# Optimization experiments

Hardware: AMD Instinct MI355X
Metric: run time of the kernel (lower is better)

## Reference

```python
import jax, jax.numpy as jnp
import numpy as np

EPS = 1e-5
NUM_HEADS = 16


def _layernorm(x, g, b):
    mu = jnp.mean(x, axis=-1, keepdims=True)
    var = jnp.mean(jnp.square(x - mu), axis=-1, keepdims=True)
    return (x - mu) * jax.lax.rsqrt(var + EPS) * g + b


def setup_inputs() -> dict:
    key = jax.random.key(0)
    ks = jax.random.split(key, 8)
    B, N, D, Hid = 2, 2048, 1024, 4096
    s = 0.02
    return {
        "x": jax.random.normal(ks[0], (B, N, D), dtype=jnp.float32),
        "w_qkv": jax.random.normal(ks[1], (D, 3 * D), dtype=jnp.float32) * s,
        "b_qkv": jnp.zeros((3 * D,), dtype=jnp.float32),
        "ln_g": jnp.ones((D,), dtype=jnp.float32),
        "ln_b": jnp.zeros((D,), dtype=jnp.float32),
        "w1": jax.random.normal(ks[2], (D, Hid), dtype=jnp.float32) * s,
        "b1": jnp.zeros((Hid,), dtype=jnp.float32),
        "w2": jax.random.normal(ks[3], (Hid, D), dtype=jnp.float32) * s,
        "b2": jnp.zeros((D,), dtype=jnp.float32),
    }


def reference(x, w_qkv, b_qkv, ln_g, ln_b, w1, b1, w2, b2):
    B, N, D = x.shape
    H = NUM_HEADS
    Dh = D // H

    # --- attention branch (pre-norm, shared LayerNorm params) ---
    xn = _layernorm(x, ln_g, ln_b)
    qkv = xn @ w_qkv + b_qkv                       # [B, N, 3D]
    qkv = qkv.reshape(B, N, 3, H, Dh).transpose(2, 0, 3, 1, 4)  # [3, B, H, N, Dh]
    q, k, v = qkv[0], qkv[1], qkv[2]
    # NOTE: original module applies NO 1/sqrt(Dh) scaling
    att = jax.nn.softmax(jnp.einsum('bhqd,bhkd->bhqk', q, k), axis=-1)
    o = jnp.einsum('bhqk,bhkd->bhqd', att, v)      # [B, H, N, Dh]
    # Faithful to source: raw reshape of [B, H, N, Dh] -> [B, N, D]
    # (the original code does NOT transpose heads back before merging)
    attn_out = o.reshape(B, N, D)
    x = x + attn_out

    # --- MLP branch ---
    xn2 = _layernorm(x, ln_g, ln_b)
    h = jax.nn.gelu(xn2 @ w1 + b1, approximate=False)
    mlp_out = h @ w2 + b2
    return x + mlp_out
```

## Files before the change

### kernel.cpp

```cpp
#include <hip/hip_runtime.h>
#include <cstdint>
#include <math.h>

typedef __attribute__((ext_vector_type(4))) float f32x4;
typedef __attribute__((ext_vector_type(8))) short bf16x8;
typedef unsigned short u16;
typedef __attribute__((ext_vector_type(4))) unsigned short u16x4;

#define LOG2E 1.44269504088896340736f

__device__ __forceinline__ u16 f2bf(float f) {
  uint32_t u = __builtin_bit_cast(uint32_t, f);
  u += 0x7FFFu + ((u >> 16) & 1u);
  return (u16)(u >> 16);
}

__device__ __forceinline__ void g2lds16(const void* g, void* l) {
  __builtin_amdgcn_global_load_lds((const __attribute__((address_space(1))) void*)g,
                                   (__attribute__((address_space(3))) void*)l, 16, 0, 0);
}

__device__ __forceinline__ float qsum16(float v) {
  v += __shfl_xor(v, 1);
  v += __shfl_xor(v, 2);
  v += __shfl_xor(v, 4);
  v += __shfl_xor(v, 8);
  return v;
}
__device__ __forceinline__ float wsum64(float v) {
  #pragma unroll
  for (int m = 32; m > 0; m >>= 1) v += __shfl_xor(v, m);
  return v;
}

__global__ void __launch_bounds__(256) transpose_f32_bf16(
    const float* __restrict__ in, u16* __restrict__ out, int R, int C) {
  __shared__ float tile[32][33];
  const int bx = blockIdx.x, by = blockIdx.y;
  const int tx = threadIdx.x & 31, ty = threadIdx.x >> 5;
  #pragma unroll
  for (int j = 0; j < 4; ++j)
    tile[ty + j * 8][tx] = in[(size_t)(by * 32 + ty + j * 8) * C + bx * 32 + tx];
  __syncthreads();
  #pragma unroll
  for (int j = 0; j < 4; ++j)
    out[(size_t)(bx * 32 + ty + j * 8) * R + by * 32 + tx] = f2bf(tile[tx][ty + j * 8]);
}

__global__ void __launch_bounds__(256) ln_kernel(
    const float* __restrict__ x, const float* __restrict__ g,
    const float* __restrict__ b, u16* __restrict__ out) {
  __shared__ float red[8];
  const int row = blockIdx.x, t = threadIdx.x, w = t >> 6;
  const float4 v = ((const float4*)(x + (size_t)row * 1024))[t];
  float s = v.x + v.y + v.z + v.w;
  s = wsum64(s);
  if ((t & 63) == 0) red[w] = s;
  __syncthreads();
  const float mean = (red[0] + red[1] + red[2] + red[3]) * (1.0f / 1024.0f);
  const float dx = v.x - mean, dy = v.y - mean, dz = v.z - mean, dw = v.w - mean;
  float s2 = dx * dx + dy * dy + dz * dz + dw * dw;
  s2 = wsum64(s2);
  if ((t & 63) == 0) red[4 + w] = s2;
  __syncthreads();
  const float rstd = rsqrtf((red[4] + red[5] + red[6] + red[7]) * (1.0f / 1024.0f) + 1e-5f);
  const float4 gv = ((const float4*)g)[t];
  const float4 bv = ((const float4*)b)[t];
  u16x4 o;
  o.x = f2bf(dx * rstd * gv.x + bv.x);
  o.y = f2bf(dy * rstd * gv.y + bv.y);
  o.z = f2bf(dz * rstd * gv.z + bv.z);
  o.w = f2bf(dw * rstd * gv.w + bv.w);
  ((u16x4*)(out + (size_t)row * 1024))[t] = o;
}

template <int EPI>
__global__ void __launch_bounds__(256, 2) gemm_bt(
    const u16* __restrict__ A, const u16* __restrict__ Bt,
    const float* __restrict__ bias, int M, int N, int K,
    u16* __restrict__ ob) {
  __shared__ u16 As[128 * 32];
  __shared__ u16 Bs[128 * 32];
  const int t = threadIdx.x;
  const int w = t >> 6, l = t & 63;
  const int lq = l >> 4, lr = l & 15;
  const int sw = (lr >> 1) & 3;
  const int wm = w >> 1, wn = w & 1;
  const int row0 = blockIdx.x * 128, col0 = blockIdx.y * 128;
  f32x4 acc[4][4] = {};
  for (int k0 = 0; k0 < K; k0 += 32) {
    #pragma unroll
    for (int i = 0; i < 2; ++i) {
      int c = i * 256 + t;
      int row = c >> 2, cl = (c & 3) ^ ((row >> 1) & 3);
      g2lds16(A + (size_t)(row0 + row) * K + k0 + cl * 8,
              (char*)As + (i * 256 + w * 64) * 16);
    }
    #pragma unroll
    for (int i = 0; i < 2; ++i) {
      int c = i * 256 + t;
      int row = c >> 2, cl = (c & 3) ^ ((row >> 1) & 3);
      g2lds16(Bt + (size_t)(col0 + row) * K + k0 + cl * 8,
              (char*)Bs + (i * 256 + w * 64) * 16);
    }
    __syncthreads();
    bf16x8 af[4], bf[4];
    #pragma unroll
    for (int tm = 0; tm < 4; ++tm)
      af[tm] = *(const bf16x8*)&As[(wm * 64 + tm * 16 + lr) * 32 + (lq ^ sw) * 8];
    #pragma unroll
    for (int tn = 0; tn < 4; ++tn)
      bf[tn] = *(const bf16x8*)&Bs[(wn * 64 + tn * 16 + lr) * 32 + (lq ^ sw) * 8];
    #pragma unroll
    for (int tm = 0; tm < 4; ++tm)
      #pragma unroll
      for (int tn = 0; tn < 4; ++tn)
        acc[tm][tn] = __builtin_amdgcn_mfma_f32_16x16x32_bf16(af[tm], bf[tn], acc[tm][tn], 0, 0, 0);
    __syncthreads();
  }
  #pragma unroll
  for (int tm = 0; tm < 4; ++tm) {
    #pragma unroll
    for (int tn = 0; tn < 4; ++tn) {
      const int gcol = col0 + wn * 64 + tn * 16 + lr;
      const float bv = bias[gcol];
      float vals[4];
      #pragma unroll
      for (int r = 0; r < 4; ++r) vals[r] = acc[tm][tn][r] + bv;
      const int g0 = row0 + wm * 64 + tm * 16 + lq * 4;
      if (EPI == 0) {
        const int tsel = gcol >> 10, hh = (gcol >> 6) & 15, dh = gcol & 63;
        const int bb = g0 >> 11, n0 = g0 & 2047;
        if (tsel == 2) {
          u16x4 pk;
          pk.x = f2bf(vals[0]); pk.y = f2bf(vals[1]);
          pk.z = f2bf(vals[2]); pk.w = f2bf(vals[3]);
          *(u16x4*)&ob[8388608 + (size_t)((bb * 16 + hh) * 64 + dh) * 2048 + n0] = pk;
        } else {
          const float sc = (tsel == 0) ? LOG2E : 1.0f;
          const size_t base = (tsel ? 4194304u : 0u) +
                              (size_t)(bb * 16 + hh) * 2048 * 64 + dh;
          #pragma unroll
          for (int r = 0; r < 4; ++r)
            ob[base + (size_t)(n0 + r) * 64] = f2bf(vals[r] * sc);
        }
      } else {
        #pragma unroll
        for (int r = 0; r < 4; ++r) {
          const float gelu = 0.5f * vals[r] * (1.0f + erff(vals[r] * 0.70710678118654752f));
          ob[(size_t)(g0 + r) * N + gcol] = f2bf(gelu);
        }
      }
    }
  }
}

__global__ void __launch_bounds__(256) gemm2_db(
    const u16* __restrict__ A, const u16* __restrict__ Bt,
    const float* __restrict__ bias, const float* __restrict__ res,
    float* __restrict__ of) {
  __shared__ u16 As0[128 * 128], As1[128 * 128];
  __shared__ u16 Bs0[128 * 128], Bs1[128 * 128];
  const int t = threadIdx.x;
  const int w = t >> 6, l = t & 63;
  const int lq = l >> 4, lr = l & 15;
  const int sw = lr & 7;
  const int wm = w >> 1, wn = w & 1;
  const int row0 = blockIdx.x * 128, col0 = blockIdx.y * 128;
  const int K = 4096, N = 1024;

#define STAGE(kt, AS, BS)                                                  \
  {                                                                        \
    _Pragma("unroll")                                                      \
    for (int i = 0; i < 8; ++i) {                                          \
      int c = i * 256 + t;                                                 \
      int row = c >> 4, cl = (c & 15) ^ (row & 7);                         \
      g2lds16(A + (size_t)(row0 + row) * K + (kt) * 128 + cl * 8,          \
              (char*)(AS) + (i * 256 + w * 64) * 16);                      \
    }                                                                      \
    _Pragma("unroll")                                                      \
    for (int i = 0; i < 8; ++i) {                                          \
      int c = i * 256 + t;                                                 \
      int row = c >> 4, cl = (c & 15) ^ (row & 7);                         \
      g2lds16(Bt + (size_t)(col0 + row) * K + (kt) * 128 + cl * 8,         \
              (char*)(BS) + (i * 256 + w * 64) * 16);                      \
    }                                                                      \
  }

#define COMPUTE(AS, BS)                                                    \
  {                                                                        \
    _Pragma("unroll")                                                      \
    for (int kk = 0; kk < 4; ++kk) {                                       \
      bf16x8 af[4], bf[4];                                                 \
      _Pragma("unroll")                                                    \
      for (int tm = 0; tm < 4; ++tm)                                       \
        af[tm] = *(const bf16x8*)&(AS)[(wm * 64 + tm * 16 + lr) * 128 +    \
                                       (((kk * 4 + lq) ^ sw)) * 8];        \
      _Pragma("unroll")                                                    \
      for (int tn = 0; tn < 4; ++tn)                                       \
        bf[tn] = *(const bf16x8*)&(BS)[(wn * 64 + tn * 16 + lr) * 128 +    \
                                       (((kk * 4 + lq) ^ sw)) * 8];        \
      _Pragma("unroll")                                                    \
      for (int tm = 0; tm < 4; ++tm)                                       \
        _Pragma("unroll")                                                  \
        for (int tn = 0; tn < 4; ++tn)                                     \
          acc[tm][tn] = __builtin_amdgcn_mfma_f32_16x16x32_bf16(           \
              af[tm], bf[tn], acc[tm][tn], 0, 0, 0);                       \
    }                                                                      \
  }

  f32x4 acc[4][4] = {};
  STAGE(0, As0, Bs0);
  for (int kt = 0; kt < 32; kt += 2) {
    __syncthreads();
    STAGE(kt + 1, As1, Bs1);
    COMPUTE(As0, Bs0);
    __syncthreads();
    if (kt + 2 < 32) STAGE(kt + 2, As0, Bs0);
    COMPUTE(As1, Bs1);
  }
#undef STAGE
#undef COMPUTE

  #pragma unroll
  for (int tm = 0; tm < 4; ++tm) {
    #pragma unroll
    for (int tn = 0; tn < 4; ++tn) {
      const int gcol = col0 + wn * 64 + tn * 16 + lr;
      const float bv = bias[gcol];
      const int g0 = row0 + wm * 64 + tm * 16 + lq * 4;
      #pragma unroll
      for (int r = 0; r < 4; ++r) {
        const size_t idx = (size_t)(g0 + r) * N + gcol;
        of[idx] = res[idx] + acc[tm][tn][r] + bv;
      }
    }
  }
}

__global__ void __launch_bounds__(256, 2) attn_kernel(
    const u16* __restrict__ q, const u16* __restrict__ k, const u16* __restrict__ vt,
    const float* __restrict__ x, float* __restrict__ x2) {
  __shared__ u16 Ks[128 * 64];
  __shared__ u16 Vs[64 * 128];
  __shared__ u16 Ps[4][16 * 136];
  const int t = threadIdx.x, w = t >> 6, l = t & 63;
  const int lq = l >> 4, lr = l & 15;
  const int sw = lr & 7;
  const int bh = blockIdx.y, qt = blockIdx.x;
  const size_t head = (size_t)bh * (2048 * 64);
  const u16* qh = q + head;
  const u16* kh = k + head;
  const u16* vth = vt + head;

  bf16x8 qf[2][2];
  #pragma unroll
  for (int tm = 0; tm < 2; ++tm)
    #pragma unroll
    for (int kk = 0; kk < 2; ++kk)
      qf[tm][kk] = *(const bf16x8*)&qh[(size_t)(qt * 128 + w * 32 + tm * 16 + lr) * 64 + kk * 32 + lq * 8];

  f32x4 o_acc[2][4] = {};
  float rsum[2][4] = {};
  u16* const pbase = &Ps[w][lq * 544 + lr];

  for (int kt = 0; kt < 16; ++kt) {
    #pragma unroll
    for (int i = 0; i < 4; ++i) {
      int c = i * 256 + t;
      int row = c >> 3, cl = (c & 7) ^ (row & 7);
      g2lds16(kh + (size_t)(kt * 128 + row) * 64 + cl * 8,
              (char*)Ks + (i * 256 + w * 64) * 16);
    }
    #pragma unroll
    for (int i = 0; i < 4; ++i) {
      int c = i * 256 + t;
      int row = c >> 4, cl = (c & 15) ^ (row & 7);
      g2lds16(vth + (size_t)row * 2048 + kt * 128 + cl * 8,
              (char*)Vs + (i * 256 + w * 64) * 16);
    }
    __syncthreads();
    bf16x8 kf[8][2];
    #pragma unroll
    for (int tn = 0; tn < 8; ++tn)
      #pragma unroll
      for (int kk = 0; kk < 2; ++kk)
        kf[tn][kk] = *(const bf16x8*)&Ks[(tn * 16 + lr) * 64 + ((kk * 4 + lq) ^ sw) * 8];
    #pragma unroll
    for (int tm = 0; tm < 2; ++tm) {
      f32x4 s_acc[8] = {};
      #pragma unroll
      for (int tn = 0; tn < 8; ++tn)
        #pragma unroll
        for (int kk = 0; kk < 2; ++kk)
          s_acc[tn] = __builtin_amdgcn_mfma_f32_16x16x32_bf16(qf[tm][kk], kf[tn][kk], s_acc[tn], 0, 0, 0);
      #pragma unroll
      for (int tn = 0; tn < 8; ++tn)
        #pragma unroll
        for (int r = 0; r < 4; ++r) {
          const float p = __builtin_amdgcn_exp2f(s_acc[tn][r]);
          rsum[tm][r] += p;
          pbase[r * 136 + tn * 16] = (u16)(__builtin_bit_cast(uint32_t, p) >> 16);
        }
      #pragma unroll
      for (int kk2 = 0; kk2 < 4; ++kk2) {
        const bf16x8 pf = *(const bf16x8*)&Ps[w][lr * 136 + kk2 * 32 + lq * 8];
        #pragma unroll
        for (int tn = 0; tn < 4; ++tn) {
          const bf16x8 vf = *(const bf16x8*)&Vs[(tn * 16 + lr) * 128 + ((kk2 * 4 + lq) ^ sw) * 8];
          o_acc[tm][tn] = __builtin_amdgcn_mfma_f32_16x16x32_bf16(pf, vf, o_acc[tm][tn], 0, 0, 0);
        }
      }
    }
    __syncthreads();
  }
  float inv[2][4];
  #pragma unroll
  for (int tm = 0; tm < 2; ++tm)
    #pragma unroll
    for (int r = 0; r < 4; ++r)
      inv[tm][r] = 1.0f / qsum16(rsum[tm][r]);
  const int bb = bh >> 4, hh = bh & 15;
  const size_t base = (size_t)bb * 2097152 + (size_t)hh * 131072;
  #pragma unroll
  for (int tm = 0; tm < 2; ++tm)
    #pragma unroll
    for (int tn = 0; tn < 4; ++tn)
      #pragma unroll
      for (int r = 0; r < 4; ++r) {
        const int n = qt * 128 + w * 32 + tm * 16 + lq * 4 + r;
        const int dh = tn * 16 + lr;
        const size_t idx = base + (size_t)n * 64 + dh;
        x2[idx] = x[idx] + o_acc[tm][tn][r] * inv[tm][r];
      }
}

extern "C" void kernel_launch(void* const* d_in, const int* in_sizes, int n_in,
                              void* d_out, int out_size, void* d_ws, size_t ws_size,
                              hipStream_t stream) {
  const float* x     = (const float*)d_in[0];
  const float* w_qkv = (const float*)d_in[1];
  const float* b_qkv = (const float*)d_in[2];
  const float* ln_g  = (const float*)d_in[3];
  const float* ln_b  = (const float*)d_in[4];
  const float* w1    = (const float*)d_in[5];
  const float* b1    = (const float*)d_in[6];
  const float* w2    = (const float*)d_in[7];
  const float* b2    = (const float*)d_in[8];
  float* out = (float*)d_out;
  char* ws = (char*)d_ws;

  u16*  wqkvT = (u16*)(ws + 0);
  u16*  qb    = (u16*)(ws + 6291456);
  u16*  xn    = (u16*)(ws + 31457280);
  u16*  h     = (u16*)(ws + 0);
  float* x2   = (float*)(ws + 39845888);
  u16*  w1T   = (u16*)(ws + 56623104);
  u16*  w2T   = (u16*)(ws + 65011712);
  u16*  xn2   = (u16*)(ws + 73400320);

  transpose_f32_bf16<<<dim3(3072 / 32, 1024 / 32), 256, 0, stream>>>(w_qkv, wqkvT, 1024, 3072);
  transpose_f32_bf16<<<dim3(4096 / 32, 1024 / 32), 256, 0, stream>>>(w1, w1T, 1024, 4096);
  transpose_f32_bf16<<<dim3(1024 / 32, 4096 / 32), 256, 0, stream>>>(w2, w2T, 4096, 1024);

  ln_kernel<<<4096, 256, 0, stream>>>(x, ln_g, ln_b, xn);
  gemm_bt<0><<<dim3(32, 24), 256, 0, stream>>>(xn, wqkvT, b_qkv, 4096, 3072, 1024, qb);
  attn_kernel<<<dim3(16, 32), 256, 0, stream>>>(qb, qb + 4194304, qb + 8388608, x, x2);
  ln_kernel<<<4096, 256, 0, stream>>>(x2, ln_g, ln_b, xn2);
  gemm_bt<1><<<dim3(32, 32), 256, 0, stream>>>(xn2, w1T, b1, 4096, 4096, 1024, h);
  gemm2_db<<<dim3(32, 8), 256, 0, stream>>>(h, w2T, b2, x2, out);
}
```

Measured before the change: 318.8 us.

## Double-buffer K/V tiles in attention kernel with smaller 64-key tiles

The attention loop now works on 64-key tiles instead of 128 and keeps two LDS buffers for K and V. The next tile's async global-to-LDS loads are issued before computing on the current one, so load latency overlaps MFMA and exp work. The P scratch row stride changes from 136 to 132, and P is read back as two 8-byte loads. This costs more barriers per key, and smaller tiles mean less work between each synchronisation.

```diff
diff --git a/kernel.cpp b/kernel.cpp
--- a/kernel.cpp
+++ b/kernel.cpp
@@ -4,6 +4,7 @@
 
 typedef __attribute__((ext_vector_type(4))) float f32x4;
 typedef __attribute__((ext_vector_type(8))) short bf16x8;
+typedef __attribute__((ext_vector_type(4))) short s16x4;
 typedef unsigned short u16;
 typedef __attribute__((ext_vector_type(4))) unsigned short u16x4;
 
@@ -241,9 +242,9 @@
 __global__ void __launch_bounds__(256, 2) attn_kernel(
     const u16* __restrict__ q, const u16* __restrict__ k, const u16* __restrict__ vt,
     const float* __restrict__ x, float* __restrict__ x2) {
-  __shared__ u16 Ks[128 * 64];
-  __shared__ u16 Vs[64 * 128];
-  __shared__ u16 Ps[4][16 * 136];
+  __shared__ u16 Ks0[64 * 64], Ks1[64 * 64];
+  __shared__ u16 Vs0[64 * 64], Vs1[64 * 64];
+  __shared__ u16 Ps[4][16 * 132];
   const int t = threadIdx.x, w = t >> 6, l = t & 63;
   const int lq = l >> 4, lr = l & 15;
   const int sw = lr & 7;
@@ -262,58 +263,79 @@
 
   f32x4 o_acc[2][4] = {};
   float rsum[2][4] = {};
-  u16* const pbase = &Ps[w][lq * 544 + lr];
-
-  for (int kt = 0; kt < 16; ++kt) {
-    #pragma unroll
-    for (int i = 0; i < 4; ++i) {
-      int c = i * 256 + t;
-      int row = c >> 3, cl = (c & 7) ^ (row & 7);
-      g2lds16(kh + (size_t)(kt * 128 + row) * 64 + cl * 8,
-              (char*)Ks + (i * 256 + w * 64) * 16);
-    }
-    #pragma unroll
-    for (int i = 0; i < 4; ++i) {
-      int c = i * 256 + t;
-      int row = c >> 4, cl = (c & 15) ^ (row & 7);
-      g2lds16(vth + (size_t)row * 2048 + kt * 128 + cl * 8,
-              (char*)Vs + (i * 256 + w * 64) * 16);
-    }
-    __syncthreads();
-    bf16x8 kf[8][2];
-    #pragma unroll
-    for (int tn = 0; tn < 8; ++tn)
-      #pragma unroll
-      for (int kk = 0; kk < 2; ++kk)
-        kf[tn][kk] = *(const bf16x8*)&Ks[(tn * 16 + lr) * 64 + ((kk * 4 + lq) ^ sw) * 8];
-    #pragma unroll
-    for (int tm = 0; tm < 2; ++tm) {
-      f32x4 s_acc[8] = {};
-      #pragma unroll
-      for (int tn = 0; tn < 8; ++tn)
-        #pragma unroll
-        for (int kk = 0; kk < 2; ++kk)
-          s_acc[tn] = __builtin_amdgcn_mfma_f32_16x16x32_bf16(qf[tm][kk], kf[tn][kk], s_acc[tn], 0, 0, 0);
-      #pragma unroll
-      for (int tn = 0; tn < 8; ++tn)
-        #pragma unroll
-        for (int r = 0; r < 4; ++r) {
-          const float p = __builtin_amdgcn_exp2f(s_acc[tn][r]);
-          rsum[tm][r] += p;
-          pbase[r * 136 + tn * 16] = (u16)(__builtin_bit_cast(uint32_t, p) >> 16);
-        }
-      #pragma unroll
-      for (int kk2 = 0; kk2 < 4; ++kk2) {
-        const bf16x8 pf = *(const bf16x8*)&Ps[w][lr * 136 + kk2 * 32 + lq * 8];
-        #pragma unroll
-        for (int tn = 0; tn < 4; ++tn) {
-          const bf16x8 vf = *(const bf16x8*)&Vs[(tn * 16 + lr) * 128 + ((kk2 * 4 + lq) ^ sw) * 8];
-          o_acc[tm][tn] = __builtin_amdgcn_mfma_f32_16x16x32_bf16(pf, vf, o_acc[tm][tn], 0, 0, 0);
-        }
-      }
-    }
-    __syncthreads();
-  }
+  u16* const pstore = &Ps[w][lq * 528 + lr];
+  const u16* const Psw = Ps[w];
+
+#define STAGE_KV(kt, KS, VS)                                                \
+  {                                                                         \
+    _Pragma("unroll")                                                       \
+    for (int i = 0; i < 2; ++i) {                                           \
+      int c = i * 256 + t;                                                  \
+      int row = c >> 3, cl = (c & 7) ^ (row & 7);                           \
+      g2lds16(kh + (size_t)((kt) * 64 + row) * 64 + cl * 8,                 \
+              (char*)(KS) + (i * 256 + w * 64) * 16);                       \
+      g2lds16(vth + (size_t)row * 2048 + (kt) * 64 + cl * 8,                \
+              (char*)(VS) + (i * 256 + w * 64) * 16);                       \
+    }                                                                       \
+  }
+
+#define COMPUTE_KV(KS, VS)                                                  \
+  {                                                                         \
+    bf16x8 kf[4][2];                                                        \
+    _Pragma("unroll")                                                       \
+    for (int tn = 0; tn < 4; ++tn)                                          \
+      _Pragma("unroll")                                                     \
+      for (int kk = 0; kk < 2; ++kk)                                        \
+        kf[tn][kk] = *(const bf16x8*)&(KS)[(tn * 16 + lr) * 64 +            \
+                                           ((kk * 4 + lq) ^ sw) * 8];       \
+    _Pragma("unroll")                                                       \
+    for (int tm = 0; tm < 2; ++tm) {                                        \
+      f32x4 s_acc[4] = {};                                                  \
+      _Pragma("unroll")                                                     \
+      for (int tn = 0; tn < 4; ++tn)                                        \
+        _Pragma("unroll")                                                   \
+        for (int kk = 0; kk < 2; ++kk)                                      \
+          s_acc[tn] = __builtin_amdgcn_mfma_f32_16x16x32_bf16(              \
+              qf[tm][kk], kf[tn][kk], s_acc[tn], 0, 0, 0);                  \
+      _Pragma("unroll")                                                     \
+      for (int tn = 0; tn < 4; ++tn)                                        \
+        _Pragma("unroll")                                                   \
+        for (int r = 0; r < 4; ++r) {                                       \
+          const float p = __builtin_amdgcn_exp2f(s_acc[tn][r]);             \
+          rsum[tm][r] += p;                                                 \
+          pstore[r * 132 + tn * 16] =                                       \
+              (u16)(__builtin_bit_cast(uint32_t, p) >> 16);                 \
+        }                                                                   \
+      _Pragma("unroll")                                                     \
+      for (int kk2 = 0; kk2 < 2; ++kk2) {                                   \
+        const int pe = lr * 132 + kk2 * 32 + lq * 8;                        \
+        const s16x4 p0 = *(const s16x4*)&Psw[pe];                           \
+        const s16x4 p1 = *(const s16x4*)&Psw[pe + 4];                       \
+        const bf16x8 pf =                                                   \
+            __builtin_shufflevector(p0, p1, 0, 1, 2, 3, 4, 5, 6, 7);        \
+        _Pragma("unroll")                                                   \
+        for (int tn = 0; tn < 4; ++tn) {                                    \
+          const bf16x8 vf = *(const bf16x8*)&(VS)[(tn * 16 + lr) * 64 +     \
+                                                  ((kk2 * 4 + lq) ^ sw) * 8]; \
+          o_acc[tm][tn] = __builtin_amdgcn_mfma_f32_16x16x32_bf16(          \
+              pf, vf, o_acc[tm][tn], 0, 0, 0);                              \
+        }                                                                   \
+      }                                                                     \
+    }                                                                       \
+  }
+
+  STAGE_KV(0, Ks0, Vs0);
+  for (int kt = 0; kt < 32; kt += 2) {
+    __syncthreads();
+    STAGE_KV(kt + 1, Ks1, Vs1);
+    COMPUTE_KV(Ks0, Vs0);
+    __syncthreads();
+    if (kt + 2 < 32) STAGE_KV(kt + 2, Ks0, Vs0);
+    COMPUTE_KV(Ks1, Vs1);
+  }
+#undef STAGE_KV
+#undef COMPUTE_KV
+
   float inv[2][4];
   #pragma unroll
   for (int tm = 0; tm < 2; ++tm)
```

Result: faster. 311.5 us (-2.3%).
